# Optimization experiments

Hardware: AMD Instinct MI355X
Metric: run time of the kernel (lower is better)

## Reference

```python
import jax, jax.numpy as jnp
import numpy as np


def diff_x(inp, r):
    left = inp[:, :, r:2 * r + 1]
    middle = inp[:, :, 2 * r + 1:] - inp[:, :, :-2 * r - 1]
    right = inp[:, :, -1:] - inp[:, :, -2 * r - 1:-r - 1]
    return jnp.concatenate([left, middle, right], axis=2)


def diff_y(inp, r):
    left = inp[:, :, :, r:2 * r + 1]
    middle = inp[:, :, :, 2 * r + 1:] - inp[:, :, :, :-2 * r - 1]
    right = inp[:, :, :, -1:] - inp[:, :, :, -2 * r - 1:-r - 1]
    return jnp.concatenate([left, middle, right], axis=3)


def setup_inputs() -> dict:
    key = jax.random.key(0)
    B, C, H, W = 8, 3, 1080, 1920
    x = jax.random.normal(key, (B, C, H, W), dtype=jnp.float32)
    return {"x": x, "r": 4}


def reference(x, r):
    # Box filter: cumsum + sliced diff along H, then along W.
    return diff_y(jnp.cumsum(diff_x(jnp.cumsum(x, axis=2), r), axis=3), r)
```

## Files before the change

### kernel.cpp

```cpp
#include <hip/hip_runtime.h>


#define W_IMG 1920
#define H_IMG 1080
#define SH 27
#define R 4

typedef float f4 __attribute__((ext_vector_type(4)));

#define ROW_BODY(JJ, DO_PREFETCH)                                         \
    {                                                                     \
        const int row = row0 + chunk + (JJ) + R;        \
        f4 v = st[JJ];                                                    \
        if (DO_PREFETCH) {                         \
            const int nrc = min(row + 9, H_IMG - 1);                      \
            st[JJ] = *(const f4*)(pcol + (long)nrc * W_IMG);              \
        }                                                                 \
        if (row >= H_IMG || !colOK) v = (f4){0.f, 0.f, 0.f, 0.f};         \
        vs += v;                                                          \
        ring[((JJ) + 8) % 9] = v;                                         \
                                                                          \
                \
        const float s3 = vs.w;                              \
        const float s2 = vs.z + s3;                                       \
        const float s1 = vs.y + s2;                                       \
        const float S  = vs.x + s1;                       \
        const float p2 = vs.x + vs.y;                       \
        const float p3 = p2 + vs.z;                                       \
                                                                          \
        const float T  = __shfl_down(S, 1);        \
        const float q1 = __shfl_down(vs.x, 2);    \
        const float q2 = __shfl_down(p2, 2);                              \
        const float q3 = __shfl_down(p3, 2);                              \
        const float q4 = __shfl_down(S, 2);                               \
                                                                          \
        f4 h;                                                             \
        h.x = S  + T + q1;                                                \
        h.y = s1 + T + q2;                                                \
        h.z = s2 + T + q3;                                                \
        h.w = s3 + T + q4;                                                \
        if (stOK) __builtin_nontemporal_store(h, (f4*)po);                \
        po += W_IMG;                                                      \
        vs -= ring[JJ];                           \
    }

__global__ void __launch_bounds__(256, 5)
box9_wave4(const float* __restrict__ x, float* __restrict__ out) {
    const int lane  = threadIdx.x & 63;
    const int wv    = threadIdx.x >> 6;
    const int strip = blockIdx.x * 4 + wv;
    const int seg   = blockIdx.y;
    const int img   = blockIdx.z;
    const long base = (long)img * (H_IMG * W_IMG);

    const int  cin_raw = strip * 240 - 4 + 4 * lane;
    const int  cin     = min(max(cin_raw, 0), W_IMG - 4);
    const bool colOK   = (cin_raw >= 0) && (cin_raw + 3 < W_IMG);
    const int  cout    = strip * 240 + 4 * lane;
    const bool stOK    = (lane < 60);

    const int row0 = seg * SH;
    const float* pcol = x + base + cin;
    float* po = out + base + (long)row0 * W_IMG + cout;

    f4 ring[9];
    f4 st[9];
    f4 vs = {0.f, 0.f, 0.f, 0.f};

#pragma unroll
    for (int t = 0; t < 8; ++t) {
        const int rc = max(row0 - R + t, 0);
        ring[t] = *(const f4*)(pcol + (long)rc * W_IMG);
    }
#pragma unroll
    for (int j = 0; j < 9; ++j) {
        const int rc = min(row0 + j + R, H_IMG - 1);
        st[j] = *(const f4*)(pcol + (long)rc * W_IMG);
    }
    __builtin_amdgcn_sched_barrier(0);
#pragma unroll
    for (int t = 0; t < 8; ++t) {
        const int row = row0 - R + t;
        f4 v = ring[t];
        if (row < 0 || !colOK) v = (f4){0.f, 0.f, 0.f, 0.f};
        ring[t] = v;
        vs += v;
    }

#pragma unroll 1
    for (int chunk = 0; chunk < SH - 9; chunk += 9) {
#pragma unroll
        for (int j = 0; j < 9; ++j) ROW_BODY(j, true);
        __builtin_amdgcn_sched_barrier(0);
    }
    {
        const int chunk = SH - 9;
#pragma unroll
        for (int j = 0; j < 9; ++j) ROW_BODY(j, false);
    }
}

extern "C" void kernel_launch(void* const* d_in, const int* in_sizes, int n_in,
                              void* d_out, int out_size, void* d_ws, size_t ws_size,
                              hipStream_t stream) {
    const float* x = (const float*)d_in[0];
    float* out = (float*)d_out;
    dim3 grid(2, 40, 24);
    box9_wave4<<<grid, 256, 0, stream>>>(x, out);
}
```

Baseline: 347.7 us.

## Replace register ring buffer with re-read of leaving rows to cut registers

Drops the 9-entry register ring and the 9-deep prefetch array. The vertical running sum now reloads the row leaving the window from global memory, which should mostly hit in cache, and processes two output rows per iteration. Launch bounds rise from 5 to 8 blocks per CU to raise occupancy. In exchange each row issues twice the global loads, and the deep explicit prefetch pipeline is lost, so latency hiding now depends on occupancy.

```diff
diff --git a/kernel.cpp b/kernel.cpp
--- a/kernel.cpp
+++ b/kernel.cpp
@@ -8,32 +8,19 @@
 
 typedef float f4 __attribute__((ext_vector_type(4)));
 
-#define ROW_BODY(JJ, DO_PREFETCH)                                         \
+#define HOUT()                                                            \
     {                                                                     \
-        const int row = row0 + chunk + (JJ) + R;        \
-        f4 v = st[JJ];                                                    \
-        if (DO_PREFETCH) {                         \
-            const int nrc = min(row + 9, H_IMG - 1);                      \
-            st[JJ] = *(const f4*)(pcol + (long)nrc * W_IMG);              \
-        }                                                                 \
-        if (row >= H_IMG || !colOK) v = (f4){0.f, 0.f, 0.f, 0.f};         \
-        vs += v;                                                          \
-        ring[((JJ) + 8) % 9] = v;                                         \
-                                                                          \
-                \
         const float s3 = vs.w;                              \
         const float s2 = vs.z + s3;                                       \
         const float s1 = vs.y + s2;                                       \
         const float S  = vs.x + s1;                       \
         const float p2 = vs.x + vs.y;                       \
         const float p3 = p2 + vs.z;                                       \
-                                                                          \
         const float T  = __shfl_down(S, 1);        \
         const float q1 = __shfl_down(vs.x, 2);    \
         const float q2 = __shfl_down(p2, 2);                              \
         const float q3 = __shfl_down(p3, 2);                              \
         const float q4 = __shfl_down(S, 2);                               \
-                                                                          \
         f4 h;                                                             \
         h.x = S  + T + q1;                                                \
         h.y = s1 + T + q2;                                                \
@@ -41,10 +28,9 @@
         h.w = s3 + T + q4;                                                \
         if (stOK) __builtin_nontemporal_store(h, (f4*)po);                \
         po += W_IMG;                                                      \
-        vs -= ring[JJ];                           \
     }
 
-__global__ void __launch_bounds__(256, 5)
+__global__ void __launch_bounds__(256, 8)
 box9_wave4(const float* __restrict__ x, float* __restrict__ out) {
     const int lane  = threadIdx.x & 63;
     const int wv    = threadIdx.x >> 6;
@@ -63,40 +49,51 @@
     const float* pcol = x + base + cin;
     float* po = out + base + (long)row0 * W_IMG + cout;
 
-    f4 ring[9];
-    f4 st[9];
     f4 vs = {0.f, 0.f, 0.f, 0.f};
+    const f4 zero = {0.f, 0.f, 0.f, 0.f};
 
+    {
+        f4 w[9];
 #pragma unroll
-    for (int t = 0; t < 8; ++t) {
-        const int rc = max(row0 - R + t, 0);
-        ring[t] = *(const f4*)(pcol + (long)rc * W_IMG);
-    }
+        for (int t = 0; t < 9; ++t) {
+            const int row = row0 - R + t;
+            const int rc  = min(max(row, 0), H_IMG - 1);
+            w[t] = *(const f4*)(pcol + (long)rc * W_IMG);
+        }
 #pragma unroll
-    for (int j = 0; j < 9; ++j) {
-        const int rc = min(row0 + j + R, H_IMG - 1);
-        st[j] = *(const f4*)(pcol + (long)rc * W_IMG);
-    }
-    __builtin_amdgcn_sched_barrier(0);
-#pragma unroll
-    for (int t = 0; t < 8; ++t) {
-        const int row = row0 - R + t;
-        f4 v = ring[t];
-        if (row < 0 || !colOK) v = (f4){0.f, 0.f, 0.f, 0.f};
-        ring[t] = v;
-        vs += v;
+        for (int t = 0; t < 9; ++t) {
+            const int row = row0 - R + t;
+            f4 v = w[t];
+            if (row < 0 || !colOK) v = zero;
+            vs += v;
+        }
+        HOUT();
     }
 
-#pragma unroll 1
-    for (int chunk = 0; chunk < SH - 9; chunk += 9) {
-#pragma unroll
-        for (int j = 0; j < 9; ++j) ROW_BODY(j, true);
-        __builtin_amdgcn_sched_barrier(0);
-    }
-    {
-        const int chunk = SH - 9;
-#pragma unroll
-        for (int j = 0; j < 9; ++j) ROW_BODY(j, false);
+#pragma unroll 2
+    for (int j = 1; j < SH; j += 2) {
+        const int r    = row0 + j;
+        const int rin0 = r + R;
+        const int rin1 = r + R + 1;
+        const int rd0  = r - R - 1;
+        const int rd1  = r - R;
+
+        f4 a = *(const f4*)(pcol + (long)min(rin0, H_IMG - 1) * W_IMG);
+        f4 b = *(const f4*)(pcol + (long)max(rd0, 0) * W_IMG);
+        f4 c = *(const f4*)(pcol + (long)min(rin1, H_IMG - 1) * W_IMG);
+        f4 d = *(const f4*)(pcol + (long)max(rd1, 0) * W_IMG);
+
+        if (rin0 >= H_IMG || !colOK) a = zero;
+        if (rd0 < 0      || !colOK) b = zero;
+        vs += a;
+        vs -= b;
+        HOUT();
+
+        if (rin1 >= H_IMG || !colOK) c = zero;
+        if (rd1 < 0      || !colOK) d = zero;
+        vs += c;
+        vs -= d;
+        HOUT();
     }
 }
 
```

Result: slower. 357.2 us (+2.7%).
